# Optimization experiments

Hardware: AMD Instinct MI355X
Metric: run time of the kernel (lower is better)

## Reference

```python
import jax, jax.numpy as jnp
import numpy as np

N, E, IN, H, OUT, K = 50000, 800000, 128, 128, 40, 10
ALPHA, EPS, AH = 0.1, 1e-5, 64


def setup_inputs() -> dict:
    key = jax.random.key(0)
    ks = jax.random.split(key, 32)
    rn = lambda k, s, sc=0.05: jax.random.normal(k, s, jnp.float32) * sc
    return dict(
        x=jax.random.normal(ks[0], (N, IN), jnp.float32),
        edge_index=jax.random.randint(ks[1], (2, E), 0, N, jnp.int64),
        edge_weight=jax.random.uniform(ks[2], (E,), jnp.float32),
        lin1_w=rn(ks[3], (H, IN)), lin1_b=rn(ks[4], (H,)),
        bn1_g=jnp.ones((H,), jnp.float32), bn1_b=jnp.zeros((H,), jnp.float32),
        bn1_m=rn(ks[5], (H,)), bn1_v=jax.random.uniform(ks[6], (H,), jnp.float32, 0.5, 1.5),
        lin2_w=rn(ks[7], (H, H)), lin2_b=rn(ks[8], (H,)),
        bn2_g=jnp.ones((H,), jnp.float32), bn2_b=jnp.zeros((H,), jnp.float32),
        bn2_m=rn(ks[9], (H,)), bn2_v=jax.random.uniform(ks[10], (H,), jnp.float32, 0.5, 1.5),
        att1_w=rn(ks[11], (AH, 2 * H)), att1_b=rn(ks[12], (AH,)),
        att2_w=rn(ks[13], (K + 1, AH)), att2_b=rn(ks[14], (K + 1,)),
        head1_w=rn(ks[15], (H // 2, H)), head1_b=rn(ks[16], (H // 2,)),
        bn3_g=jnp.ones((H // 2,), jnp.float32), bn3_b=jnp.zeros((H // 2,), jnp.float32),
        bn3_m=rn(ks[17], (H // 2,)), bn3_v=jax.random.uniform(ks[18], (H // 2,), jnp.float32, 0.5, 1.5),
        head2_w=rn(ks[19], (OUT, H // 2)), head2_b=rn(ks[20], (OUT,)),
    )


def _bn(x, g, b, m, v):
    # eval-mode BatchNorm1d with running stats
    return (x - m) * jax.lax.rsqrt(v + EPS) * g + b


def reference(x, edge_index, edge_weight,
              lin1_w, lin1_b, bn1_g, bn1_b, bn1_m, bn1_v,
              lin2_w, lin2_b, bn2_g, bn2_b, bn2_m, bn2_v,
              att1_w, att1_b, att2_w, att2_b,
              head1_w, head1_b, bn3_g, bn3_b, bn3_m, bn3_v,
              head2_w, head2_b):
    row, col = edge_index[0], edge_index[1]

    # dense stem (dropout is identity in eval mode)
    h = jax.nn.relu(_bn(x @ lin1_w.T + lin1_b, bn1_g, bn1_b, bn1_m, bn1_v))
    identity = h
    h = jax.nn.relu(_bn(h @ lin2_w.T + lin2_b, bn2_g, bn2_b, bn2_m, bn2_v)) + identity
    base = h  # h0 for APPNP

    # edge normalization (loop-invariant): w_e / clamp(sum_w(row), 1)
    wsum = jnp.clip(jax.ops.segment_sum(edge_weight, row, num_segments=N), 1.0)
    enorm = edge_weight / wsum[row]  # [E]

    xs = [h]
    for _ in range(K):  # fixed K iterations of gather -> scatter-add
        agg = jax.ops.segment_sum(h[row] * enorm[:, None], col, num_segments=N)
        h = (1.0 - ALPHA) * agg + ALPHA * base
        xs.append(h)

    stacked = jnp.stack(xs, axis=-1)                    # [N, H, K+1]
    ctx = jnp.concatenate([xs[0], xs[-1]], axis=-1)     # [N, 2H]
    a = jax.nn.gelu(ctx @ att1_w.T + att1_b, approximate=False) @ att2_w.T + att2_b
    w = jax.nn.softmax(a, axis=-1)[:, None, :]          # [N, 1, K+1]
    fused = (stacked * w).sum(axis=-1)                  # [N, H]

    z = jax.nn.relu(_bn(fused @ head1_w.T + head1_b, bn3_g, bn3_b, bn3_m, bn3_v))
    return z @ head2_w.T + head2_b
```

## Files before the change

kernel.cpp:

```cpp
#include <hip/hip_runtime.h>
#include <hip/hip_fp16.h>
#include <math.h>

#define NN 50000
#define EE 800000
#define HH 128
#define KIT 10
#define NHF (NN * HH)
#define CC 64
#define CH 12500
#define RRH 4
#define NRH 12500

typedef _Float16 half8 __attribute__((ext_vector_type(8)));
typedef float floatx4 __attribute__((ext_vector_type(4)));

__device__ __forceinline__ float gelu_exact(float x) {
  return 0.5f * x * (1.f + erff(x * 0.70710678118654752f));
}

__device__ __forceinline__ float4 ld4(const float* p) { return *(const float4*)p; }
__device__ __forceinline__ float4 ld4(const __half* p) {
  const __half2* q = (const __half2*)p;
  float2 lo = __half22float2(q[0]);
  float2 hi = __half22float2(q[1]);
  return make_float4(lo.x, lo.y, hi.x, hi.y);
}
__device__ __forceinline__ void st1(float* p, float v) { *p = v; }
__device__ __forceinline__ void st1(__half* p, float v) { *p = __float2half_rn(v); }

__global__ __launch_bounds__(256) void hist2_kernel(const int* __restrict__ ei,
                                                    const float* __restrict__ ew,
                                                    int* __restrict__ pdeg,
                                                    float* __restrict__ pwsum,
                                                    int* __restrict__ rank) {
  __shared__ int hist[NRH];
  const int c = blockIdx.x;
  const int z = blockIdx.y;
  const bool isdeg = (z < RRH);
  const int lo = (isdeg ? z : z - RRH) * NRH;
  for (int i = threadIdx.x; i < NRH; i += 256) hist[i] = 0;
  __syncthreads();
  const int e0 = c * CH;
  if (isdeg) {
    const int4* d4 = (const int4*)(ei + (size_t)EE + e0);
    for (int i = threadIdx.x; i < CH / 4; i += 256) {
      int4 d = d4[i];
      int e = e0 + i * 4;
      unsigned u0 = (unsigned)(d.x - lo), u1 = (unsigned)(d.y - lo);
      unsigned u2 = (unsigned)(d.z - lo), u3 = (unsigned)(d.w - lo);
      if (u0 < NRH) rank[e]     = atomicAdd(&hist[u0], 1);
      if (u1 < NRH) rank[e + 1] = atomicAdd(&hist[u1], 1);
      if (u2 < NRH) rank[e + 2] = atomicAdd(&hist[u2], 1);
      if (u3 < NRH) rank[e + 3] = atomicAdd(&hist[u3], 1);
    }
    __syncthreads();
    for (int i = threadIdx.x; i < NRH; i += 256)
      pdeg[(size_t)c * NN + lo + i] = hist[i];
  } else {
    float* whist = (float*)hist;
    const int4* s4 = (const int4*)(ei + e0);
    const float4* w4 = (const float4*)(ew + e0);
    for (int i = threadIdx.x; i < CH / 4; i += 256) {
      int4 s = s4[i];
      float4 w = w4[i];
      unsigned u0 = (unsigned)(s.x - lo), u1 = (unsigned)(s.y - lo);
      unsigned u2 = (unsigned)(s.z - lo), u3 = (unsigned)(s.w - lo);
      if (u0 < NRH) atomicAdd(&whist[u0], w.x);
      if (u1 < NRH) atomicAdd(&whist[u1], w.y);
      if (u2 < NRH) atomicAdd(&whist[u2], w.z);
      if (u3 < NRH) atomicAdd(&whist[u3], w.w);
    }
    __syncthreads();
    for (int i = threadIdx.x; i < NRH; i += 256)
      pwsum[(size_t)c * NN + lo + i] = whist[i];
  }
}

__global__ __launch_bounds__(256) void reduce_kernel(int* __restrict__ pdeg,
                                                     const float* __restrict__ pwsum,
                                                     int* __restrict__ deg,
                                                     float* __restrict__ wsum,
                                                     int* __restrict__ bsum) {
  int node = blockIdx.x * 256 + threadIdx.x;
  int acc = 0; float wacc = 0.f;
  if (node < NN) {
    for (int c = 0; c < CC; ++c) {
      size_t idx = (size_t)c * NN + node;
      int t = pdeg[idx];
      pdeg[idx] = acc;
      acc += t;
      wacc += pwsum[idx];
    }
    deg[node] = acc;
    wsum[node] = wacc;
  }
  __shared__ int red[256];
  red[threadIdx.x] = (node < NN) ? acc : 0;
  __syncthreads();
  for (int off = 128; off > 0; off >>= 1) {
    if (threadIdx.x < off) red[threadIdx.x] += red[threadIdx.x + off];
    __syncthreads();
  }
  if (threadIdx.x == 0) bsum[blockIdx.x] = red[0];
}

__global__ __launch_bounds__(256) void scan2_kernel(const int* __restrict__ bsum,
                                                    int* __restrict__ boff,
                                                    int* __restrict__ row_start, int nb, int n) {
  __shared__ int buf[256];
  int tid = threadIdx.x;
  int v = (tid < nb) ? bsum[tid] : 0;
  buf[tid] = v;
  __syncthreads();
  for (int off = 1; off < 256; off <<= 1) {
    int t = (tid >= off) ? buf[tid - off] : 0;
    __syncthreads();
    buf[tid] += t;
    __syncthreads();
  }
  if (tid < nb) boff[tid] = buf[tid] - v;
  if (tid == 255) row_start[n] = buf[255];
}

__global__ __launch_bounds__(256) void scan3_kernel(const int* __restrict__ deg,
                                                    const int* __restrict__ boff,
                                                    int* __restrict__ row_start, int n) {
  __shared__ int buf[256];
  int tid = threadIdx.x;
  int i = blockIdx.x * 256 + tid;
  int v = (i < n) ? deg[i] : 0;
  buf[tid] = v;
  __syncthreads();
  for (int off = 1; off < 256; off <<= 1) {
    int t = (tid >= off) ? buf[tid - off] : 0;
    __syncthreads();
    buf[tid] += t;
    __syncthreads();
  }
  if (i < n) row_start[i] = boff[blockIdx.x] + buf[tid] - v;
}

__global__ __launch_bounds__(256) void csr_fill_kernel(const int* __restrict__ ei,
                                                       const float* __restrict__ ew,
                                                       const float* __restrict__ wsum,
                                                       const int* __restrict__ row_start,
                                                       const int* __restrict__ pdeg_excl,
                                                       const int* __restrict__ rank,
                                                       int2* __restrict__ csr, int e_cnt) {
  int e = blockIdx.x * 256 + threadIdx.x;
  if (e >= e_cnt) return;
  int c = e / CH;
  int src = ei[e], dst = ei[EE + e];
  float ws = wsum[src];
  ws = ws < 1.f ? 1.f : ws;
  float v = 0.9f * ew[e] / ws;
  int pos = row_start[dst] + pdeg_excl[(size_t)c * NN + dst] + rank[e];
  csr[pos] = make_int2(src, __float_as_int(v));
}

__global__ __launch_bounds__(256) void prop_kernel(const __half* __restrict__ h_cur,
                                                   const __half* __restrict__ base,
                                                   const int* __restrict__ row_start,
                                                   const long* __restrict__ csr,
                                                   __half* __restrict__ h_next) {
  int node = __builtin_amdgcn_readfirstlane((int)blockIdx.x * 4 + (int)(threadIdx.x >> 6));
  if (node >= NN) return;
  int lane = threadIdx.x & 63;
  const __half2* hc = (const __half2*)h_cur;
  float2 b = __half22float2(((const __half2*)base)[(size_t)node * 64 + lane]);
  float ax = 0.1f * b.x, ay = 0.1f * b.y;
  float bx = 0.f, by = 0.f;
  int s = row_start[node], e = row_start[node + 1];
  int nfull = (e - s) >> 3;
  int i = s;
  if (nfull > 0) {
    long cur[8];
#pragma unroll
    for (int j = 0; j < 8; ++j) cur[j] = csr[i + j];
    i += 8;
    for (int bidx = 1; bidx < nfull; ++bidx) {
      long nxt[8];
#pragma unroll
      for (int j = 0; j < 8; ++j) nxt[j] = csr[i + j];
      i += 8;
      float2 g[8];
#pragma unroll
      for (int j = 0; j < 8; ++j) g[j] = __half22float2(hc[(size_t)(int)cur[j] * 64 + lane]);
#pragma unroll
      for (int j = 0; j < 8; ++j) {
        float v = __int_as_float((int)(cur[j] >> 32));
        if (j & 1) { bx = fmaf(v, g[j].x, bx); by = fmaf(v, g[j].y, by); }
        else       { ax = fmaf(v, g[j].x, ax); ay = fmaf(v, g[j].y, ay); }
      }
#pragma unroll
      for (int j = 0; j < 8; ++j) cur[j] = nxt[j];
    }
    float2 g[8];
#pragma unroll
    for (int j = 0; j < 8; ++j) g[j] = __half22float2(hc[(size_t)(int)cur[j] * 64 + lane]);
#pragma unroll
    for (int j = 0; j < 8; ++j) {
      float v = __int_as_float((int)(cur[j] >> 32));
      if (j & 1) { bx = fmaf(v, g[j].x, bx); by = fmaf(v, g[j].y, by); }
      else       { ax = fmaf(v, g[j].x, ax); ay = fmaf(v, g[j].y, ay); }
    }
  }
  for (; i < e; ++i) {
    long c0 = csr[i];
    float2 g0 = __half22float2(hc[(size_t)(int)c0 * 64 + lane]);
    float v = __int_as_float((int)(c0 >> 32));
    ax = fmaf(v, g0.x, ax); ay = fmaf(v, g0.y, ay);
  }
  ((__half2*)h_next)[(size_t)node * 64 + lane] =
      __float22half2_rn(make_float2(ax + bx, ay + by));
}

template <int K, int KA, int JP, int JR, int ACT, bool RESID, typename IT, typename OT>
__global__ __launch_bounds__(256) void mfma_dense(
    const IT* __restrict__ Xa, const IT* __restrict__ Xb,
    const float* __restrict__ W, const float* __restrict__ lb,
    const float* __restrict__ bg, const float* __restrict__ bb,
    const float* __restrict__ bm, const float* __restrict__ bv,
    const OT* __restrict__ resid, OT* __restrict__ out) {
  constexpr int KC = (K > 128) ? 128 : K;
  static_assert(K % KC == 0 && KC % 32 == 0 && JP % 16 == 0, "");
  constexpr int JT = JP / 16;
  __shared__ _Float16 xL[128][KC + 8];
  __shared__ _Float16 wL[JP][KC + 8];
  const int tid = threadIdx.x;
  const int wv = tid >> 6, lane = tid & 63;
  const int q = lane >> 4, m = lane & 15;
  const int r0 = blockIdx.x * 128;

  floatx4 acc[2][JT];
#pragma unroll
  for (int rt = 0; rt < 2; ++rt)
#pragma unroll
    for (int jt = 0; jt < JT; ++jt) acc[rt][jt] = (floatx4)(0.f);

  for (int kc = 0; kc < K; kc += KC) {
    __syncthreads();
    for (int idx = tid; idx < 128 * (KC / 4); idx += 256) {
      int r = idx / (KC / 4);
      int c4 = (idx % (KC / 4)) * 4;
      int row = r0 + r;
      int col = kc + c4;
      float4 v = make_float4(0.f, 0.f, 0.f, 0.f);
      if (row < NN) {
        if (col < KA) v = ld4(&Xa[(size_t)row * KA + col]);
        else          v = ld4(&Xb[(size_t)row * (K - KA) + (col - KA)]);
      }
      xL[r][c4 + 0] = (_Float16)v.x; xL[r][c4 + 1] = (_Float16)v.y;
      xL[r][c4 + 2] = (_Float16)v.z; xL[r][c4 + 3] = (_Float16)v.w;
    }
    for (int idx = tid; idx < JP * (KC / 4); idx += 256) {
      int j = idx / (KC / 4);
      int c4 = (idx % (KC / 4)) * 4;
      float4 v = make_float4(0.f, 0.f, 0.f, 0.f);
      if (j < JR) v = *(const float4*)&W[(size_t)j * K + kc + c4];
      wL[j][c4 + 0] = (_Float16)v.x; wL[j][c4 + 1] = (_Float16)v.y;
      wL[j][c4 + 2] = (_Float16)v.z; wL[j][c4 + 3] = (_Float16)v.w;
    }
    __syncthreads();
#pragma unroll
    for (int ks = 0; ks < KC; ks += 32) {
      half8 a0 = *(const half8*)&xL[wv * 32 + m][ks + q * 8];
      half8 a1 = *(const half8*)&xL[wv * 32 + 16 + m][ks + q * 8];
#pragma unroll
      for (int jt = 0; jt < JT; ++jt) {
        half8 b = *(const half8*)&wL[jt * 16 + m][ks + q * 8];
        acc[0][jt] = __builtin_amdgcn_mfma_f32_16x16x32_f16(a0, b, acc[0][jt], 0, 0, 0);
        acc[1][jt] = __builtin_amdgcn_mfma_f32_16x16x32_f16(a1, b, acc[1][jt], 0, 0, 0);
      }
    }
  }
#pragma unroll
  for (int jt = 0; jt < JT; ++jt) {
    int j = jt * 16 + m;
    if (j >= JR) continue;
    float sc = 0.f, sh = 0.f;
    if (ACT == 1) {
      sc = bg[j] * rsqrtf(bv[j] + 1e-5f);
      sh = (lb[j] - bm[j]) * sc + bb[j];
    } else {
      sh = lb[j];
    }
#pragma unroll
    for (int rt = 0; rt < 2; ++rt) {
#pragma unroll
      for (int reg = 0; reg < 4; ++reg) {
        int row = r0 + wv * 32 + rt * 16 + q * 4 + reg;
        if (row >= NN) continue;
        float a = acc[rt][jt][reg];
        float y;
        if (ACT == 0)      y = a + sh;
        else if (ACT == 1) y = fmaxf(fmaf(a, sc, sh), 0.f);
        else               y = gelu_exact(a + sh);
        if (RESID) y += (float)resid[(size_t)row * JR + j];
        st1(&out[(size_t)row * JR + j], y);
      }
    }
  }
}

__global__ __launch_bounds__(64) void att2_softmax_kernel(const __half* __restrict__ g,
                                                          const float* __restrict__ W2,
                                                          const float* __restrict__ b2,
                                                          float* __restrict__ attw, int n_rows) {
  __shared__ float gl[64][65];
  int r0 = blockIdx.x * 64;
  for (int idx = threadIdx.x; idx < 64 * 16; idx += 64) {
    int r = idx >> 4, c4 = (idx & 15) * 4;
    float4 v = make_float4(0.f, 0.f, 0.f, 0.f);
    if (r0 + r < n_rows) v = ld4(&g[(size_t)(r0 + r) * 64 + c4]);
    gl[r][c4] = v.x; gl[r][c4 + 1] = v.y; gl[r][c4 + 2] = v.z; gl[r][c4 + 3] = v.w;
  }
  __syncthreads();
  int r = threadIdx.x;
  int n = r0 + r;
  if (n >= n_rows) return;
  float a[KIT + 1];
#pragma unroll
  for (int j = 0; j < KIT + 1; ++j) {
    float acc = b2[j];
#pragma unroll
    for (int k = 0; k < 64; ++k) acc = fmaf(gl[r][k], W2[j * 64 + k], acc);
    a[j] = acc;
  }
  float mx = a[0];
#pragma unroll
  for (int j = 1; j < KIT + 1; ++j) mx = fmaxf(mx, a[j]);
  float s = 0.f;
#pragma unroll
  for (int j = 0; j < KIT + 1; ++j) { a[j] = expf(a[j] - mx); s += a[j]; }
  float inv = 1.f / s;
#pragma unroll
  for (int j = 0; j < KIT + 1; ++j) attw[n * 16 + j] = a[j] * inv;
}

__global__ __launch_bounds__(256) void fused_gather_kernel(const __half* __restrict__ XS,
                                                           const float* __restrict__ attw,
                                                           __half* __restrict__ fused) {
  int node = __builtin_amdgcn_readfirstlane((int)blockIdx.x * 4 + (int)(threadIdx.x >> 6));
  if (node >= NN) return;
  int lane = threadIdx.x & 63;
  float ax = 0.f, ay = 0.f;
#pragma unroll
  for (int k = 0; k <= KIT; ++k) {
    float wk = attw[node * 16 + k];
    float2 v = __half22float2(((const __half2*)(XS + (size_t)k * NHF))[(size_t)node * 64 + lane]);
    ax = fmaf(wk, v.x, ax);
    ay = fmaf(wk, v.y, ay);
  }
  ((__half2*)fused)[(size_t)node * 64 + lane] = __float22half2_rn(make_float2(ax, ay));
}

__global__ __launch_bounds__(256) void fused_accum_kernel(const __half* __restrict__ h,
                                                          const float* __restrict__ attw,
                                                          float* __restrict__ fused, int k) {
  int node = __builtin_amdgcn_readfirstlane((int)blockIdx.x * 4 + (int)(threadIdx.x >> 6));
  if (node >= NN) return;
  int lane = threadIdx.x & 63;
  float wk = attw[node * 16 + k];
  float2 v = __half22float2(((const __half2*)h)[(size_t)node * 64 + lane]);
  float2 o;
  if (k == 0) {
    o = make_float2(wk * v.x, wk * v.y);
  } else {
    float2 f = ((const float2*)fused)[(size_t)node * 64 + lane];
    o = make_float2(fmaf(wk, v.x, f.x), fmaf(wk, v.y, f.y));
  }
  ((float2*)fused)[(size_t)node * 64 + lane] = o;
}

extern "C" void kernel_launch(void* const* d_in, const int* in_sizes, int n_in,
                              void* d_out, int out_size, void* d_ws, size_t ws_size,
                              hipStream_t stream) {
  (void)in_sizes; (void)n_in; (void)out_size;
  const float* x      = (const float*)d_in[0];
  const int*   ei     = (const int*)d_in[1];
  const float* ew     = (const float*)d_in[2];
  const float* lin1_w = (const float*)d_in[3];
  const float* lin1_b = (const float*)d_in[4];
  const float* bn1_g  = (const float*)d_in[5];
  const float* bn1_b  = (const float*)d_in[6];
  const float* bn1_m  = (const float*)d_in[7];
  const float* bn1_v  = (const float*)d_in[8];
  const float* lin2_w = (const float*)d_in[9];
  const float* lin2_b = (const float*)d_in[10];
  const float* bn2_g  = (const float*)d_in[11];
  const float* bn2_b  = (const float*)d_in[12];
  const float* bn2_m  = (const float*)d_in[13];
  const float* bn2_v  = (const float*)d_in[14];
  const float* att1_w = (const float*)d_in[15];
  const float* att1_b = (const float*)d_in[16];
  const float* att2_w = (const float*)d_in[17];
  const float* att2_b = (const float*)d_in[18];
  const float* head1_w= (const float*)d_in[19];
  const float* head1_b= (const float*)d_in[20];
  const float* bn3_g  = (const float*)d_in[21];
  const float* bn3_b  = (const float*)d_in[22];
  const float* bn3_m  = (const float*)d_in[23];
  const float* bn3_v  = (const float*)d_in[24];
  const float* head2_w= (const float*)d_in[25];
  const float* head2_b= (const float*)d_in[26];
  float* out = (float*)d_out;

  char* p = (char*)d_ws;
  auto alloc = [&](size_t bytes) -> void* {
    void* r = (void*)p;
    p += (bytes + 255) & ~(size_t)255;
    return r;
  };
  int*   row_start= (int*)alloc((size_t)(NN + 1) * 4);
  int*   bsum     = (int*)alloc((size_t)256 * 4);
  int*   boff     = (int*)alloc((size_t)256 * 4);
  int*   deg      = (int*)alloc((size_t)NN * 4);
  float* wsum     = (float*)alloc((size_t)NN * 4);
  long*  csr      = (long*)alloc((size_t)EE * 8);
  __half* gbuf    = (__half*)alloc((size_t)NN * 64 * 2);
  float* attw     = (float*)alloc((size_t)NN * 16 * 4);
  __half* h1      = (__half*)alloc((size_t)NHF * 2);
  __half* fusedH  = (__half*)alloc((size_t)NHF * 2);
  __half* zbuf    = (__half*)alloc((size_t)NN * 64 * 2);
  size_t common = (size_t)(p - (char*)d_ws);
  size_t stored_need = common + (size_t)(KIT + 1) * NHF * 2 + 4096;
  bool stored = ws_size >= stored_need;

  __half* XS = nullptr;
  int* pdeg; float* pwsum; int* rank;
  if (stored) {
    XS = (__half*)alloc((size_t)(KIT + 1) * NHF * 2);
    char* ovl = (char*)(XS + (size_t)8 * NHF);
    pdeg  = (int*)ovl;
    pwsum = (float*)(ovl + (size_t)CC * NN * 4);
    rank  = (int*)(ovl + 2 * (size_t)CC * NN * 4);
  } else {
    pdeg  = (int*)alloc((size_t)CC * NN * 4);
    pwsum = (float*)alloc((size_t)CC * NN * 4);
    rank  = (int*)alloc((size_t)EE * 4);
  }

  const int GE  = (EE + 255) / 256;
  const int GN  = (NN + 255) / 256;
  const int GM  = (NN + 127) / 128;
  const int GP  = (NN + 3) / 4;
  const int GA  = (NN + 63) / 64;

  hist2_kernel<<<dim3(CC, 2 * RRH), 256, 0, stream>>>(ei, ew, pdeg, pwsum, rank);
  reduce_kernel<<<GN, 256, 0, stream>>>(pdeg, pwsum, deg, wsum, bsum);
  scan2_kernel<<<1, 256, 0, stream>>>(bsum, boff, row_start, GN, NN);
  scan3_kernel<<<GN, 256, 0, stream>>>(deg, boff, row_start, NN);
  csr_fill_kernel<<<GE, 256, 0, stream>>>(ei, ew, wsum, row_start, pdeg, rank,
                                          (int2*)csr, EE);

  if (stored) {
    mfma_dense<128, 128, 128, 128, 1, false, float, __half><<<GM, 256, 0, stream>>>(
        x, (const float*)nullptr, lin1_w, lin1_b, bn1_g, bn1_b, bn1_m, bn1_v, nullptr, h1);
    mfma_dense<128, 128, 128, 128, 1, true, __half, __half><<<GM, 256, 0, stream>>>(
        h1, (const __half*)nullptr, lin2_w, lin2_b, bn2_g, bn2_b, bn2_m, bn2_v, h1, XS);
    for (int k = 0; k < KIT; ++k) {
      prop_kernel<<<GP, 256, 0, stream>>>(XS + (size_t)k * NHF, XS, row_start,
                                          csr, XS + (size_t)(k + 1) * NHF);
    }
    mfma_dense<256, 128, 64, 64, 2, false, __half, __half><<<GM, 256, 0, stream>>>(
        XS, XS + (size_t)KIT * NHF, att1_w, att1_b, nullptr, nullptr, nullptr, nullptr,
        nullptr, gbuf);
    att2_softmax_kernel<<<GA, 64, 0, stream>>>(gbuf, att2_w, att2_b, attw, NN);
    fused_gather_kernel<<<GP, 256, 0, stream>>>(XS, attw, fusedH);
    mfma_dense<128, 128, 64, 64, 1, false, __half, __half><<<GM, 256, 0, stream>>>(
        fusedH, (const __half*)nullptr, head1_w, head1_b, bn3_g, bn3_b, bn3_m, bn3_v,
        nullptr, zbuf);
  } else {
    float*  fusedF = (float*)alloc((size_t)NHF * 4);
    __half* base   = (__half*)alloc((size_t)NHF * 2);
    __half* hA     = (__half*)alloc((size_t)NHF * 2);
    __half* hB     = (__half*)alloc((size_t)NHF * 2);
    mfma_dense<128, 128, 128, 128, 1, false, float, __half><<<GM, 256, 0, stream>>>(
        x, (const float*)nullptr, lin1_w, lin1_b, bn1_g, bn1_b, bn1_m, bn1_v, nullptr, h1);
    mfma_dense<128, 128, 128, 128, 1, true, __half, __half><<<GM, 256, 0, stream>>>(
        h1, (const __half*)nullptr, lin2_w, lin2_b, bn2_g, bn2_b, bn2_m, bn2_v, h1, base);
    const __half* cur = base;
    for (int k = 1; k <= KIT; ++k) {
      __half* nxt = (k & 1) ? hA : hB;
      prop_kernel<<<GP, 256, 0, stream>>>(cur, base, row_start, csr, nxt);
      cur = nxt;
    }
    mfma_dense<256, 128, 64, 64, 2, false, __half, __half><<<GM, 256, 0, stream>>>(
        base, cur, att1_w, att1_b, nullptr, nullptr, nullptr, nullptr, nullptr, gbuf);
    att2_softmax_kernel<<<GA, 64, 0, stream>>>(gbuf, att2_w, att2_b, attw, NN);
    fused_accum_kernel<<<GP, 256, 0, stream>>>(base, attw, fusedF, 0);
    cur = base;
    for (int k = 1; k <= KIT; ++k) {
      __half* nxt = (k & 1) ? hA : hB;
      prop_kernel<<<GP, 256, 0, stream>>>(cur, base, row_start, csr, nxt);
      fused_accum_kernel<<<GP, 256, 0, stream>>>(nxt, attw, fusedF, k);
      cur = nxt;
    }
    mfma_dense<128, 128, 64, 64, 1, false, float, __half><<<GM, 256, 0, stream>>>(
        fusedF, (const float*)nullptr, head1_w, head1_b, bn3_g, bn3_b, bn3_m, bn3_v,
        nullptr, zbuf);
  }

  mfma_dense<64, 64, 48, 40, 0, false, __half, float><<<GM, 256, 0, stream>>>(
      zbuf, (const __half*)nullptr, head2_w, head2_b, nullptr, nullptr, nullptr, nullptr,
      nullptr, out);
}
```

Before: 599.0 us.

## Load dense-layer A operands straight into registers and swizzle weight LDS tiles

Reworks the MFMA dense kernel so each wavefront handles a 16-row tile and loads its activation operands directly from global memory into registers, skipping the LDS staging of X. Weights are staged once in LDS across the full K with an XOR swizzle to avoid bank conflicts, and the K-chunk loop and its extra barriers are removed. The aim is to cut LDS traffic and synchronisation in the dense layers. In exchange, the weight tile is reloaded by four times as many blocks, and register pressure rises because every K slice of A is held in registers at once.

```diff
diff --git a/kernel.cpp b/kernel.cpp
--- a/kernel.cpp
+++ b/kernel.cpp
@@ -13,7 +13,10 @@
 #define NRH 12500
 
 typedef _Float16 half8 __attribute__((ext_vector_type(8)));
+typedef _Float16 half4v __attribute__((ext_vector_type(4)));
 typedef float floatx4 __attribute__((ext_vector_type(4)));
+
+static_assert(NN % 16 == 0, "row tiles must be exact");
 
 __device__ __forceinline__ float gelu_exact(float x) {
   return 0.5f * x * (1.f + erff(x * 0.70710678118654752f));
@@ -217,69 +220,85 @@
 }
 
 template <int K, int KA, int JP, int JR, int ACT, bool RESID, typename IT, typename OT>
-__global__ __launch_bounds__(256) void mfma_dense(
+__global__ __launch_bounds__(256) void mfma_dense2(
     const IT* __restrict__ Xa, const IT* __restrict__ Xb,
     const float* __restrict__ W, const float* __restrict__ lb,
     const float* __restrict__ bg, const float* __restrict__ bb,
     const float* __restrict__ bm, const float* __restrict__ bv,
     const OT* __restrict__ resid, OT* __restrict__ out) {
-  constexpr int KC = (K > 128) ? 128 : K;
-  static_assert(K % KC == 0 && KC % 32 == 0 && JP % 16 == 0, "");
+  static_assert(K % 32 == 0 && KA % 32 == 0 && JP % 16 == 0, "");
   constexpr int JT = JP / 16;
-  __shared__ _Float16 xL[128][KC + 8];
-  __shared__ _Float16 wL[JP][KC + 8];
+  constexpr int NS = K / 32;
+  constexpr bool ISF = __is_same(IT, float);
+  __shared__ _Float16 wL[JP][K];
+
   const int tid = threadIdx.x;
   const int wv = tid >> 6, lane = tid & 63;
   const int q = lane >> 4, m = lane & 15;
-  const int r0 = blockIdx.x * 128;
-
-  floatx4 acc[2][JT];
-#pragma unroll
-  for (int rt = 0; rt < 2; ++rt)
-#pragma unroll
-    for (int jt = 0; jt < JT; ++jt) acc[rt][jt] = (floatx4)(0.f);
-
-  for (int kc = 0; kc < K; kc += KC) {
-    __syncthreads();
-    for (int idx = tid; idx < 128 * (KC / 4); idx += 256) {
-      int r = idx / (KC / 4);
-      int c4 = (idx % (KC / 4)) * 4;
-      int row = r0 + r;
-      int col = kc + c4;
-      float4 v = make_float4(0.f, 0.f, 0.f, 0.f);
-      if (row < NN) {
-        if (col < KA) v = ld4(&Xa[(size_t)row * KA + col]);
-        else          v = ld4(&Xb[(size_t)row * (K - KA) + (col - KA)]);
+  const int t = blockIdx.x * 4 + wv;
+  const bool active = (t < NN / 16);
+  const int row = t * 16 + m;
+
+  half8  a[ISF ? 1 : NS];
+  float4 af0[ISF ? NS : 1], af1[ISF ? NS : 1];
+  if (active) {
+#pragma unroll
+    for (int s = 0; s < NS; ++s) {
+      int c = s * 32 + q * 8;
+      if constexpr (ISF) {
+        const float* p = (const float*)Xa + (size_t)row * K + c;
+        af0[s] = *(const float4*)p;
+        af1[s] = *(const float4*)(p + 4);
+      } else {
+        const __half* p = (c < KA) ? (const __half*)Xa + (size_t)row * KA + c
+                                   : (const __half*)Xb + (size_t)row * (K - KA) + (c - KA);
+        a[s] = *(const half8*)p;
       }
-      xL[r][c4 + 0] = (_Float16)v.x; xL[r][c4 + 1] = (_Float16)v.y;
-      xL[r][c4 + 2] = (_Float16)v.z; xL[r][c4 + 3] = (_Float16)v.w;
-    }
-    for (int idx = tid; idx < JP * (KC / 4); idx += 256) {
-      int j = idx / (KC / 4);
-      int c4 = (idx % (KC / 4)) * 4;
-      float4 v = make_float4(0.f, 0.f, 0.f, 0.f);
-      if (j < JR) v = *(const float4*)&W[(size_t)j * K + kc + c4];
-      wL[j][c4 + 0] = (_Float16)v.x; wL[j][c4 + 1] = (_Float16)v.y;
-      wL[j][c4 + 2] = (_Float16)v.z; wL[j][c4 + 3] = (_Float16)v.w;
-    }
-    __syncthreads();
-#pragma unroll
-    for (int ks = 0; ks < KC; ks += 32) {
-      half8 a0 = *(const half8*)&xL[wv * 32 + m][ks + q * 8];
-      half8 a1 = *(const half8*)&xL[wv * 32 + 16 + m][ks + q * 8];
-#pragma unroll
-      for (int jt = 0; jt < JT; ++jt) {
-        half8 b = *(const half8*)&wL[jt * 16 + m][ks + q * 8];
-        acc[0][jt] = __builtin_amdgcn_mfma_f32_16x16x32_f16(a0, b, acc[0][jt], 0, 0, 0);
-        acc[1][jt] = __builtin_amdgcn_mfma_f32_16x16x32_f16(a1, b, acc[1][jt], 0, 0, 0);
-      }
-    }
-  }
+    }
+  }
+
+  constexpr int C4 = K / 4;
+  for (int idx = tid; idx < JP * C4; idx += 256) {
+    int j = idx / C4;
+    int c4 = (idx % C4) * 4;
+    float4 v = make_float4(0.f, 0.f, 0.f, 0.f);
+    if (j < JR) v = *(const float4*)&W[(size_t)j * K + c4];
+    int cs = ((((c4 >> 3) ^ (j & 7)) << 3) | (c4 & 7));
+    *(half4v*)&wL[j][cs] = (half4v){(_Float16)v.x, (_Float16)v.y,
+                                    (_Float16)v.z, (_Float16)v.w};
+  }
+  __syncthreads();
+
+  if (!active) return;
+
+  floatx4 acc[JT];
+#pragma unroll
+  for (int jt = 0; jt < JT; ++jt) acc[jt] = (floatx4)(0.f);
+
+#pragma unroll
+  for (int s = 0; s < NS; ++s) {
+    half8 av;
+    if constexpr (ISF) {
+      float4 f0 = af0[s], f1 = af1[s];
+      av = (half8){(_Float16)f0.x, (_Float16)f0.y, (_Float16)f0.z, (_Float16)f0.w,
+                   (_Float16)f1.x, (_Float16)f1.y, (_Float16)f1.z, (_Float16)f1.w};
+    } else {
+      av = a[s];
+    }
+    int kq = s * 4 + q;
+#pragma unroll
+    for (int jt = 0; jt < JT; ++jt) {
+      int j = jt * 16 + m;
+      half8 b = *(const half8*)&wL[j][(kq ^ (j & 7)) << 3];
+      acc[jt] = __builtin_amdgcn_mfma_f32_16x16x32_f16(av, b, acc[jt], 0, 0, 0);
+    }
+  }
+
 #pragma unroll
   for (int jt = 0; jt < JT; ++jt) {
     int j = jt * 16 + m;
     if (j >= JR) continue;
-    float sc = 0.f, sh = 0.f;
+    float sc = 0.f, sh;
     if (ACT == 1) {
       sc = bg[j] * rsqrtf(bv[j] + 1e-5f);
       sh = (lb[j] - bm[j]) * sc + bb[j];
@@ -287,19 +306,15 @@
       sh = lb[j];
     }
 #pragma unroll
-    for (int rt = 0; rt < 2; ++rt) {
-#pragma unroll
-      for (int reg = 0; reg < 4; ++reg) {
-        int row = r0 + wv * 32 + rt * 16 + q * 4 + reg;
-        if (row >= NN) continue;
-        float a = acc[rt][jt][reg];
-        float y;
-        if (ACT == 0)      y = a + sh;
-        else if (ACT == 1) y = fmaxf(fmaf(a, sc, sh), 0.f);
-        else               y = gelu_exact(a + sh);
-        if (RESID) y += (float)resid[(size_t)row * JR + j];
-        st1(&out[(size_t)row * JR + j], y);
-      }
+    for (int reg = 0; reg < 4; ++reg) {
+      int r = t * 16 + q * 4 + reg;
+      float aa = acc[jt][reg];
+      float y;
+      if (ACT == 0)      y = aa + sh;
+      else if (ACT == 1) y = fmaxf(fmaf(aa, sc, sh), 0.f);
+      else               y = gelu_exact(aa + sh);
+      if (RESID) y += (float)resid[(size_t)r * JR + j];
+      st1(&out[(size_t)r * JR + j], y);
     }
   }
 }
@@ -444,7 +459,7 @@
 
   const int GE  = (EE + 255) / 256;
   const int GN  = (NN + 255) / 256;
-  const int GM  = (NN + 127) / 128;
+  const int GT  = (NN / 16 + 3) / 4;
   const int GP  = (NN + 3) / 4;
   const int GA  = (NN + 63) / 64;
 
@@ -456,20 +471,20 @@
                                           (int2*)csr, EE);
 
   if (stored) {
-    mfma_dense<128, 128, 128, 128, 1, false, float, __half><<<GM, 256, 0, stream>>>(
+    mfma_dense2<128, 128, 128, 128, 1, false, float, __half><<<GT, 256, 0, stream>>>(
         x, (const float*)nullptr, lin1_w, lin1_b, bn1_g, bn1_b, bn1_m, bn1_v, nullptr, h1);
-    mfma_dense<128, 128, 128, 128, 1, true, __half, __half><<<GM, 256, 0, stream>>>(
+    mfma_dense2<128, 128, 128, 128, 1, true, __half, __half><<<GT, 256, 0, stream>>>(
         h1, (const __half*)nullptr, lin2_w, lin2_b, bn2_g, bn2_b, bn2_m, bn2_v, h1, XS);
     for (int k = 0; k < KIT; ++k) {
       prop_kernel<<<GP, 256, 0, stream>>>(XS + (size_t)k * NHF, XS, row_start,
                                           csr, XS + (size_t)(k + 1) * NHF);
     }
-    mfma_dense<256, 128, 64, 64, 2, false, __half, __half><<<GM, 256, 0, stream>>>(
+    mfma_dense2<256, 128, 64, 64, 2, false, __half, __half><<<GT, 256, 0, stream>>>(
         XS, XS + (size_t)KIT * NHF, att1_w, att1_b, nullptr, nullptr, nullptr, nullptr,
         nullptr, gbuf);
     att2_softmax_kernel<<<GA, 64, 0, stream>>>(gbuf, att2_w, att2_b, attw, NN);
     fused_gather_kernel<<<GP, 256, 0, stream>>>(XS, attw, fusedH);
-    mfma_dense<128, 128, 64, 64, 1, false, __half, __half><<<GM, 256, 0, stream>>>(
+    mfma_dense2<128, 128, 64, 64, 1, false, __half, __half><<<GT, 256, 0, stream>>>(
         fusedH, (const __half*)nullptr, head1_w, head1_b, bn3_g, bn3_b, bn3_m, bn3_v,
         nullptr, zbuf);
   } else {
@@ -477,9 +492,9 @@
     __half* base   = (__half*)alloc((size_t)NHF * 2);
     __half* hA     = (__half*)alloc((size_t)NHF * 2);
     __half* hB     = (__half*)alloc((size_t)NHF * 2);
-    mfma_dense<128, 128, 128, 128, 1, false, float, __half><<<GM, 256, 0, stream>>>(
+    mfma_dense2<128, 128, 128, 128, 1, false, float, __half><<<GT, 256, 0, stream>>>(
         x, (const float*)nullptr, lin1_w, lin1_b, bn1_g, bn1_b, bn1_m, bn1_v, nullptr, h1);
-    mfma_dense<128, 128, 128, 128, 1, true, __half, __half><<<GM, 256, 0, stream>>>(
+    mfma_dense2<128, 128, 128, 128, 1, true, __half, __half><<<GT, 256, 0, stream>>>(
         h1, (const __half*)nullptr, lin2_w, lin2_b, bn2_g, bn2_b, bn2_m, bn2_v, h1, base);
     const __half* cur = base;
     for (int k = 1; k <= KIT; ++k) {
@@ -487,7 +502,7 @@
       prop_kernel<<<GP, 256, 0, stream>>>(cur, base, row_start, csr, nxt);
       cur = nxt;
     }
-    mfma_dense<256, 128, 64, 64, 2, false, __half, __half><<<GM, 256, 0, stream>>>(
+    mfma_dense2<256, 128, 64, 64, 2, false, __half, __half><<<GT, 256, 0, stream>>>(
         base, cur, att1_w, att1_b, nullptr, nullptr, nullptr, nullptr, nullptr, gbuf);
     att2_softmax_kernel<<<GA, 64, 0, stream>>>(gbuf, att2_w, att2_b, attw, NN);
     fused_accum_kernel<<<GP, 256, 0, stream>>>(base, attw, fusedF, 0);
@@ -498,12 +513,12 @@
       fused_accum_kernel<<<GP, 256, 0, stream>>>(nxt, attw, fusedF, k);
       cur = nxt;
     }
-    mfma_dense<128, 128, 64, 64, 1, false, float, __half><<<GM, 256, 0, stream>>>(
+    mfma_dense2<128, 128, 64, 64, 1, false, float, __half><<<GT, 256, 0, stream>>>(
         fusedF, (const float*)nullptr, head1_w, head1_b, bn3_g, bn3_b, bn3_m, bn3_v,
         nullptr, zbuf);
   }
 
-  mfma_dense<64, 64, 48, 40, 0, false, __half, float><<<GM, 256, 0, stream>>>(
+  mfma_dense2<64, 64, 48, 40, 0, false, __half, float><<<GT, 256, 0, stream>>>(
       zbuf, (const __half*)nullptr, head2_w, head2_b, nullptr, nullptr, nullptr, nullptr,
       nullptr, out);
 }
```

Measured after the change: 574.4 us. -4.1%, faster.
